# Optimization experiments

Measured on AMD Instinct MI355X. Metric: run time of the kernel, lower is better.

Reference implementation:

```python
import jax, jax.numpy as jnp
import numpy as np

B, S, D_MODEL = 2, 1024, 3072
HEADS, HEAD_DIM = 24, 128
EPS = 1e-6


def _rms_norm(x, w):
    # RMSNorm over last dim (head_dim), elementwise affine
    var = jnp.mean(jnp.square(x), axis=-1, keepdims=True)
    return x * jax.lax.rsqrt(var + EPS) * w


def _apply_rotary(x, freqs_cis):
    # x: [B, S, H, D]; freqs_cis: [S, 1, rot_dim] broadcasting over B via leading dims
    rot_dim = freqs_cis.shape[-1]
    xr, x_pass = x[..., :rot_dim], x[..., rot_dim:]
    cos_ = jnp.cos(freqs_cis).astype(x.dtype)
    sin_ = jnp.sin(freqs_cis).astype(x.dtype)
    x1, x2 = jnp.split(xr, 2, axis=-1)
    x_rot = jnp.concatenate((-x2, x1), axis=-1)
    return jnp.concatenate((xr * cos_ + x_rot * sin_, x_pass), axis=-1)


def setup_inputs() -> dict:
    key = jax.random.key(0)
    ks = jax.random.split(key, 8)
    inner = HEADS * HEAD_DIM
    scale = 1.0 / np.sqrt(D_MODEL)
    return {
        "hidden_states": jax.random.normal(ks[0], (B, S, D_MODEL), dtype=jnp.float32),
        "image_rotary_emb": jax.random.uniform(ks[1], (S, 1, HEAD_DIM), dtype=jnp.float32) * 6.283,
        "Wq": jax.random.normal(ks[2], (inner, D_MODEL), dtype=jnp.float32) * scale,
        "Wk": jax.random.normal(ks[3], (inner, D_MODEL), dtype=jnp.float32) * scale,
        "Wv": jax.random.normal(ks[4], (inner, D_MODEL), dtype=jnp.float32) * scale,
        "Wo": jax.random.normal(ks[5], (D_MODEL, inner), dtype=jnp.float32) * scale,
        "norm_q_w": jnp.ones((HEAD_DIM,), dtype=jnp.float32),
        "norm_k_w": jnp.ones((HEAD_DIM,), dtype=jnp.float32),
    }


def reference(hidden_states, image_rotary_emb, Wq, Wk, Wv, Wo, norm_q_w, norm_k_w):
    # QKV projections: [B,S,Dm] @ [Dm,inner] -> [B,S,H,Dh]
    q = jnp.einsum("bsd,ed->bse", hidden_states, Wq).reshape(B, S, HEADS, HEAD_DIM)
    k = jnp.einsum("bsd,ed->bse", hidden_states, Wk).reshape(B, S, HEADS, HEAD_DIM)
    v = jnp.einsum("bsd,ed->bse", hidden_states, Wv).reshape(B, S, HEADS, HEAD_DIM)
    # per-head RMSNorm on q/k
    q = _rms_norm(q, norm_q_w)
    k = _rms_norm(k, norm_k_w)
    # RoPE (Megatron rotate_half, full head dim rotated)
    q = _apply_rotary(q, image_rotary_emb)
    k = _apply_rotary(k, image_rotary_emb)
    # SDPA (non-causal, no mask): [B,H,S,S]
    scale = 1.0 / np.sqrt(HEAD_DIM)
    scores = jnp.einsum("bqhd,bkhd->bhqk", q, k) * scale
    attn = jax.nn.softmax(scores, axis=-1)
    out = jnp.einsum("bhqk,bkhd->bqhd", attn, v).reshape(B, S, HEADS * HEAD_DIM)
    return jnp.einsum("bse,de->bsd", out, Wo)
```

## Files before the change

kernel.cpp:

```cpp
#include <hip/hip_runtime.h>
#include <hip/hip_bf16.h>
#include <math.h>

#define B_   2
#define S_   1024
#define DM_  3072
#define H_   24
#define HD_  128
#define BH_  (B_*H_)
#define KDIM 3072
#define QSCALE 0.08838834764831845f

typedef __attribute__((ext_vector_type(8))) short short8;
typedef __attribute__((ext_vector_type(4))) float f32x4;

__device__ __forceinline__ unsigned short f2bf(float f) {
    union { float f; unsigned u; } v; v.f = f;
    unsigned r = v.u + 0x7fffu + ((v.u >> 16) & 1u);
    return (unsigned short)(r >> 16);
}

#define GLD_LDS16(gptr, ldsptr)                                                            \
    __builtin_amdgcn_global_load_lds(                                                      \
        (const __attribute__((address_space(1))) unsigned int*)(gptr),                     \
        (__attribute__((address_space(3))) unsigned int*)(ldsptr), 16, 0, 0)

#define SEG0 1572864
#define SEGW 2359296
#define SB1  (SEG0 + SEGW)
#define SB2  (SB1 + SEGW)
#define SB3  (SB2 + SEGW)
#define SB4  (SB3 + SEGW)
#define SB5  (SB4 + 32768)
#define CVT_BLOCKS 43136

__global__ __launch_bounds__(256) void cvt_all(const float* __restrict__ hs,
                                               const float* __restrict__ Wq,
                                               const float* __restrict__ Wk,
                                               const float* __restrict__ Wv,
                                               const float* __restrict__ Wo,
                                               const float* __restrict__ freqs,
                                               unsigned short* __restrict__ Xb,
                                               unsigned short* __restrict__ Wqkvb,
                                               unsigned short* __restrict__ Wob,
                                               float2* __restrict__ tab) {
    int i = blockIdx.x * 256 + threadIdx.x;
    const float* src;
    unsigned short* dst;
    int j;
    if (i < SEG0)      { src = hs; dst = Xb;              j = i; }
    else if (i < SB1)  { src = Wq; dst = Wqkvb;           j = i - SEG0; }
    else if (i < SB2)  { src = Wk; dst = Wqkvb + 9437184; j = i - SB1; }
    else if (i < SB3)  { src = Wv; dst = Wqkvb + 18874368; j = i - SB2; }
    else if (i < SB4)  { src = Wo; dst = Wob;             j = i - SB3; }
    else {
        j = i - SB4;
        float4 f = ((const float4*)freqs)[j];
        float4 lo = make_float4(cosf(f.x), sinf(f.x), cosf(f.y), sinf(f.y));
        float4 hi = make_float4(cosf(f.z), sinf(f.z), cosf(f.w), sinf(f.w));
        ((float4*)tab)[2 * j]     = lo;
        ((float4*)tab)[2 * j + 1] = hi;
        return;
    }
    float4 v = ((const float4*)src)[j];
    ushort4 o;
    o.x = f2bf(v.x); o.y = f2bf(v.y); o.z = f2bf(v.z); o.w = f2bf(v.w);
    ((ushort4*)dst)[j] = o;
}

template <int FUSED>
__global__ __launch_bounds__(256) void gemm_fused(const unsigned short* __restrict__ A,
                                                  const unsigned short* __restrict__ Bm,
                                                  float* __restrict__ C, int Ndim,
                                                  const float2* __restrict__ rtab,
                                                  const float* __restrict__ nqw,
                                                  const float* __restrict__ nkw,
                                                  unsigned short* __restrict__ Qb,
                                                  unsigned short* __restrict__ Kb,
                                                  unsigned short* __restrict__ Vtb) {
    __shared__ __align__(16) unsigned short As[128 * 64];
    __shared__ __align__(16) unsigned short Bs[128 * 64];
    __shared__ float pse[4][64];
    const int t = threadIdx.x;
    const int bx = blockIdx.x;
    const int m0 = blockIdx.y * 128, n0 = bx * 128;
    const int w = t >> 6, lane = t & 63, quad = lane >> 4, ln = lane & 15;
    const int wm = (w >> 1) * 64;
    const int p = w & 1;
    const int dj0 = p ? 32 : 0;
    const int rl = lane >> 3;
    const int gc = (lane & 7) ^ rl;
    const int cs = ln & 7;
    const int woff = (w == 1) ? 32 : (w == 2) ? -32 : 0;

    f32x4 acc[4][4];
#pragma unroll
    for (int i = 0; i < 4; ++i)
#pragma unroll
        for (int j = 0; j < 4; ++j) acc[i][j] = (f32x4){0.f, 0.f, 0.f, 0.f};

    const unsigned short* ga = &A[(long long)(m0 + w * 32 + rl) * KDIM + gc * 8];
    const unsigned short* gb = &Bm[(long long)(n0 + w * 32 + woff + rl) * KDIM + gc * 8];

    for (int kt = 0; kt < KDIM / 64; ++kt) {
#pragma unroll
        for (int c = 0; c < 4; ++c) {
            const int r0 = w * 32 + c * 8;
            GLD_LDS16(ga + (long long)(c * 8) * KDIM, &As[r0 * 64]);
            GLD_LDS16(gb + (long long)(c * 8) * KDIM, &Bs[r0 * 64]);
        }
        ga += 64; gb += 64;
        __syncthreads();
#pragma unroll
        for (int ks = 0; ks < 2; ++ks) {
            short8 a[4], b[4];
#pragma unroll
            for (int i = 0; i < 4; ++i) {
                int row = wm + i * 16 + ln;
                a[i] = *(const short8*)&As[row * 64 + (((ks * 4 + quad) ^ cs) << 3)];
            }
#pragma unroll
            for (int j = 0; j < 4; ++j) {
                int row = p * 64 + j * 16 + ln;
                b[j] = *(const short8*)&Bs[row * 64 + (((ks * 4 + quad) ^ cs) << 3)];
            }
#pragma unroll
            for (int i = 0; i < 4; ++i)
#pragma unroll
                for (int j = 0; j < 4; ++j)
                    acc[i][j] = __builtin_amdgcn_mfma_f32_16x16x32_bf16(a[i], b[j], acc[i][j], 0, 0, 0);
        }
        __syncthreads();
    }

    if (!FUSED) {
#pragma unroll
        for (int i = 0; i < 4; ++i)
#pragma unroll
            for (int reg = 0; reg < 4; ++reg) {
                int row = m0 + wm + i * 16 + quad * 4 + reg;
                float* crow = C + (long long)row * Ndim + n0 + ln;
                crow[dj0]      = acc[i][0][reg];
                crow[dj0 + 16] = acc[i][1][reg];
                crow[dj0 + 64] = acc[i][2][reg];
                crow[dj0 + 80] = acc[i][3][reg];
            }
        return;
    }
    const int region = bx / 24;
    const int h = bx % 24;
    if (region < 2) {
#pragma unroll
        for (int i = 0; i < 4; ++i)
#pragma unroll
            for (int reg = 0; reg < 4; ++reg) {
                float s = 0.f;
#pragma unroll
                for (int j = 0; j < 4; ++j) { float v = acc[i][j][reg]; s += v * v; }
#pragma unroll
                for (int off = 8; off; off >>= 1) s += __shfl_xor(s, off, 16);
                if (ln == 0) pse[w][i * 16 + quad * 4 + reg] = s;
            }
        __syncthreads();
        const float* nw = region ? nkw : nqw;
        unsigned short* outp = region ? Kb : Qb;
        const float scl = region ? 1.f : QSCALE;
        const float nw0  = nw[dj0 + ln],      nw1  = nw[dj0 + 16 + ln];
        const float nw64 = nw[dj0 + 64 + ln], nw80 = nw[dj0 + 80 + ln];
#pragma unroll
        for (int i = 0; i < 4; ++i)
#pragma unroll
            for (int reg = 0; reg < 4; ++reg) {
                const int idx = i * 16 + quad * 4 + reg;
                const float tot = pse[w][idx] + pse[w ^ 1][idx];
                const float rr = rsqrtf(tot * (1.f / 128.f) + 1e-6f);
                const int row = m0 + wm + idx;
                const int b = row >> 10, s = row & 1023;
                const long long ob = ((long long)(b * H_ + h) * S_ + s) * HD_;
                {
                    const int d1 = dj0 + ln;
                    float y1 = acc[i][0][reg] * rr * nw0;
                    float y2 = acc[i][2][reg] * rr * nw64;
                    float2 c1 = rtab[s * HD_ + d1], c2 = rtab[s * HD_ + d1 + 64];
                    outp[ob + d1]      = f2bf((y1 * c1.x - y2 * c1.y) * scl);
                    outp[ob + d1 + 64] = f2bf((y2 * c2.x + y1 * c2.y) * scl);
                }
                {
                    const int d1 = dj0 + 16 + ln;
                    float y1 = acc[i][1][reg] * rr * nw1;
                    float y2 = acc[i][3][reg] * rr * nw80;
                    float2 c1 = rtab[s * HD_ + d1], c2 = rtab[s * HD_ + d1 + 64];
                    outp[ob + d1]      = f2bf((y1 * c1.x - y2 * c1.y) * scl);
                    outp[ob + d1 + 64] = f2bf((y2 * c2.x + y1 * c2.y) * scl);
                }
            }
    } else {
#pragma unroll
        for (int i = 0; i < 4; ++i)
#pragma unroll
            for (int reg = 0; reg < 4; ++reg) {
                const int row = m0 + wm + i * 16 + quad * 4 + reg;
                const int b = row >> 10, s = row & 1023;
                const long long vb = (long long)(b * H_ + h) * HD_;
#pragma unroll
                for (int j = 0; j < 4; ++j) {
                    const int d = dj0 + (j & 1) * 16 + (j >> 1) * 64 + ln;
                    Vtb[(vb + d) * S_ + s] = f2bf(acc[i][j][reg]);
                }
            }
    }
}

__global__ __launch_bounds__(256) void attn(const unsigned short* __restrict__ Qb,
                                            const unsigned short* __restrict__ Kb,
                                            const unsigned short* __restrict__ Vtb,
                                            unsigned short* __restrict__ Ob) {
    __shared__ __align__(16) unsigned short Ks[64 * 128];
    __shared__ __align__(16) unsigned short Vts[128 * 64];
    __shared__ __align__(16) unsigned short Ps[4][16][72];
    const int bh = blockIdx.x, qt = blockIdx.y;
    const int t = threadIdx.x, w = t >> 6, lane = t & 63, quad = lane >> 4, ln = lane & 15;
    const int b = bh / H_, h = bh - b * H_;

    short8 qfrag[4];
    const long long qbase = ((long long)bh * S_ + qt * 64 + w * 16 + ln) * HD_;
#pragma unroll
    for (int ks = 0; ks < 4; ++ks)
        qfrag[ks] = *(const short8*)&Qb[qbase + ks * 32 + quad * 8];

    f32x4 o[8];
#pragma unroll
    for (int n = 0; n < 8; ++n) o[n] = (f32x4){0.f, 0.f, 0.f, 0.f};
    float l_run[4] = {0.f, 0.f, 0.f, 0.f};

    const int krow_l = lane >> 4, ksl = lane & 15;
    const int vrow_l = lane >> 3, vsl = lane & 7;

    for (int kt = 0; kt < S_ / 64; ++kt) {
        __syncthreads();
#pragma unroll
        for (int c = 0; c < 4; ++c) {
            {
                const int r = c * 16 + w * 4 + krow_l;
                const int gcn = ksl ^ (r & 15);
                GLD_LDS16(&Kb[((long long)bh * S_ + kt * 64 + r) * HD_ + gcn * 8],
                          &Ks[(c * 16 + w * 4) * 128]);
            }
            {
                const int r = c * 32 + w * 8 + vrow_l;
                const int gcn = vsl ^ (r & 7);
                GLD_LDS16(&Vtb[((long long)bh * HD_ + r) * S_ + kt * 64 + gcn * 8],
                          &Vts[(c * 32 + w * 8) * 64]);
            }
        }
        __syncthreads();
        f32x4 sj[4];
#pragma unroll
        for (int j = 0; j < 4; ++j) {
            f32x4 sa = (f32x4){0.f, 0.f, 0.f, 0.f};
#pragma unroll
            for (int ks = 0; ks < 4; ++ks) {
                const int row = j * 16 + ln;
                const int slot = (ks * 4 + quad) ^ (row & 15);
                short8 bb = *(const short8*)&Ks[row * 128 + slot * 8];
                sa = __builtin_amdgcn_mfma_f32_16x16x32_bf16(qfrag[ks], bb, sa, 0, 0, 0);
            }
            sj[j] = sa;
        }
#pragma unroll
        for (int r = 0; r < 4; ++r) {
            float sum = 0.f;
#pragma unroll
            for (int j = 0; j < 4; ++j) {
                float p = __expf(sj[j][r]);
                sj[j][r] = p;
                sum += p;
            }
#pragma unroll
            for (int off = 8; off; off >>= 1) sum += __shfl_xor(sum, off, 16);
            l_run[r] += sum;
        }
#pragma unroll
        for (int j = 0; j < 4; ++j)
#pragma unroll
            for (int r = 0; r < 4; ++r)
                Ps[w][quad * 4 + r][j * 16 + ln] = f2bf(sj[j][r]);
        __asm__ volatile("s_waitcnt lgkmcnt(0)" ::: "memory");
#pragma unroll
        for (int ks = 0; ks < 2; ++ks) {
            short8 pf = *(const short8*)&Ps[w][ln][ks * 32 + quad * 8];
#pragma unroll
            for (int n = 0; n < 8; ++n) {
                const int row = n * 16 + ln;
                const int slot = (ks * 4 + quad) ^ (row & 7);
                short8 vf = *(const short8*)&Vts[row * 64 + slot * 8];
                o[n] = __builtin_amdgcn_mfma_f32_16x16x32_bf16(pf, vf, o[n], 0, 0, 0);
            }
        }
    }
    float inv[4];
#pragma unroll
    for (int r = 0; r < 4; ++r) inv[r] = 1.f / l_run[r];
    const int row_s = qt * 64 + w * 16 + quad * 4;
#pragma unroll
    for (int n = 0; n < 8; ++n)
#pragma unroll
        for (int r = 0; r < 4; ++r) {
            long long off = ((long long)b * S_ + row_s + r) * DM_ + h * HD_ + n * 16 + ln;
            Ob[off] = f2bf(o[n][r] * inv[r]);
        }
}

extern "C" void kernel_launch(void* const* d_in, const int* in_sizes, int n_in,
                              void* d_out, int out_size, void* d_ws, size_t ws_size,
                              hipStream_t stream) {
    const float* hs    = (const float*)d_in[0];
    const float* freqs = (const float*)d_in[1];
    const float* Wq    = (const float*)d_in[2];
    const float* Wk    = (const float*)d_in[3];
    const float* Wv    = (const float*)d_in[4];
    const float* Wo    = (const float*)d_in[5];
    const float* nqw   = (const float*)d_in[6];
    const float* nkw   = (const float*)d_in[7];
    float* out = (float*)d_out;

    char* ws = (char*)d_ws;
    unsigned short* Xb    = (unsigned short*)(ws);
    unsigned short* Wqkvb = (unsigned short*)(ws + 12582912LL);
    unsigned short* Wob   = (unsigned short*)(ws + 69206016LL);
    unsigned short* Qb    = (unsigned short*)(ws + 88080384LL);
    unsigned short* Kb    = (unsigned short*)(ws + 100663296LL);
    unsigned short* Vtb   = (unsigned short*)(ws + 113246208LL);
    unsigned short* Ob    = (unsigned short*)(ws + 125829120LL);
    float2*         rtab  = (float2*)        (ws + 138412032LL);

    cvt_all<<<CVT_BLOCKS, 256, 0, stream>>>(hs, Wq, Wk, Wv, Wo, freqs,
                                            Xb, Wqkvb, Wob, rtab);
    gemm_fused<1><<<dim3(72, 16), 256, 0, stream>>>(Xb, Wqkvb, nullptr, 0,
                                                    rtab, nqw, nkw, Qb, Kb, Vtb);
    attn<<<dim3(BH_, S_ / 64), 256, 0, stream>>>(Qb, Kb, Vtb, Ob);
    gemm_fused<0><<<dim3(24, 16), 256, 0, stream>>>(Ob, Wob, out, DM_,
                                                    nullptr, nullptr, nullptr,
                                                    nullptr, nullptr, nullptr);
}
```

Measured before the change: 454.4 us.

## Swap grid axes for L2 reuse and use a 64-row tile for the output GEMM

Splits the templated GEMM into a QKV kernel and a separate output-projection kernel. The QKV and attention grids are transposed so consecutive blocks share the same weight tile or the same batch-head, which should improve L2 reuse of B rows and K/V. The output GEMM uses a 64x128 tile giving 768 blocks instead of 384, which fills the CUs better, at the cost of lower per-block arithmetic intensity.

```diff
diff --git a/kernel.cpp b/kernel.cpp
--- a/kernel.cpp
+++ b/kernel.cpp
@@ -68,22 +68,20 @@
     ((ushort4*)dst)[j] = o;
 }
 
-template <int FUSED>
-__global__ __launch_bounds__(256) void gemm_fused(const unsigned short* __restrict__ A,
-                                                  const unsigned short* __restrict__ Bm,
-                                                  float* __restrict__ C, int Ndim,
-                                                  const float2* __restrict__ rtab,
-                                                  const float* __restrict__ nqw,
-                                                  const float* __restrict__ nkw,
-                                                  unsigned short* __restrict__ Qb,
-                                                  unsigned short* __restrict__ Kb,
-                                                  unsigned short* __restrict__ Vtb) {
+__global__ __launch_bounds__(256) void gemm_qkv(const unsigned short* __restrict__ A,
+                                                const unsigned short* __restrict__ Bm,
+                                                const float2* __restrict__ rtab,
+                                                const float* __restrict__ nqw,
+                                                const float* __restrict__ nkw,
+                                                unsigned short* __restrict__ Qb,
+                                                unsigned short* __restrict__ Kb,
+                                                unsigned short* __restrict__ Vtb) {
     __shared__ __align__(16) unsigned short As[128 * 64];
     __shared__ __align__(16) unsigned short Bs[128 * 64];
     __shared__ float pse[4][64];
     const int t = threadIdx.x;
-    const int bx = blockIdx.x;
-    const int m0 = blockIdx.y * 128, n0 = bx * 128;
+    const int bx = blockIdx.y;
+    const int m0 = blockIdx.x * 128, n0 = bx * 128;
     const int w = t >> 6, lane = t & 63, quad = lane >> 4, ln = lane & 15;
     const int wm = (w >> 1) * 64;
     const int p = w & 1;
@@ -133,20 +131,6 @@
         __syncthreads();
     }
 
-    if (!FUSED) {
-#pragma unroll
-        for (int i = 0; i < 4; ++i)
-#pragma unroll
-            for (int reg = 0; reg < 4; ++reg) {
-                int row = m0 + wm + i * 16 + quad * 4 + reg;
-                float* crow = C + (long long)row * Ndim + n0 + ln;
-                crow[dj0]      = acc[i][0][reg];
-                crow[dj0 + 16] = acc[i][1][reg];
-                crow[dj0 + 64] = acc[i][2][reg];
-                crow[dj0 + 80] = acc[i][3][reg];
-            }
-        return;
-    }
     const int region = bx / 24;
     const int h = bx % 24;
     if (region < 2) {
@@ -211,6 +195,69 @@
     }
 }
 
+__global__ __launch_bounds__(256) void gemm_out(const unsigned short* __restrict__ A,
+                                                const unsigned short* __restrict__ Bm,
+                                                float* __restrict__ C, int Ndim) {
+    __shared__ __align__(16) unsigned short As[64 * 64];
+    __shared__ __align__(16) unsigned short Bs[128 * 64];
+    const int t = threadIdx.x;
+    const int m0 = blockIdx.x * 64, n0 = blockIdx.y * 128;
+    const int w = t >> 6, lane = t & 63, quad = lane >> 4, ln = lane & 15;
+    const int wm = (w >> 1) * 32, wn = (w & 1) * 64;
+    const int rl = lane >> 3;
+    const int gc = (lane & 7) ^ rl;
+    const int cs = ln & 7;
+
+    f32x4 acc[2][4];
+#pragma unroll
+    for (int i = 0; i < 2; ++i)
+#pragma unroll
+        for (int j = 0; j < 4; ++j) acc[i][j] = (f32x4){0.f, 0.f, 0.f, 0.f};
+
+    const unsigned short* ga = &A[(long long)(m0 + w * 16 + rl) * KDIM + gc * 8];
+    const unsigned short* gb = &Bm[(long long)(n0 + w * 32 + rl) * KDIM + gc * 8];
+
+    for (int kt = 0; kt < KDIM / 64; ++kt) {
+#pragma unroll
+        for (int c = 0; c < 2; ++c)
+            GLD_LDS16(ga + (long long)(c * 8) * KDIM, &As[(w * 16 + c * 8) * 64]);
+#pragma unroll
+        for (int c = 0; c < 4; ++c)
+            GLD_LDS16(gb + (long long)(c * 8) * KDIM, &Bs[(w * 32 + c * 8) * 64]);
+        ga += 64; gb += 64;
+        __syncthreads();
+#pragma unroll
+        for (int ks = 0; ks < 2; ++ks) {
+            short8 a[2], b[4];
+#pragma unroll
+            for (int i = 0; i < 2; ++i) {
+                int row = wm + i * 16 + ln;
+                a[i] = *(const short8*)&As[row * 64 + (((ks * 4 + quad) ^ cs) << 3)];
+            }
+#pragma unroll
+            for (int j = 0; j < 4; ++j) {
+                int row = wn + j * 16 + ln;
+                b[j] = *(const short8*)&Bs[row * 64 + (((ks * 4 + quad) ^ cs) << 3)];
+            }
+#pragma unroll
+            for (int i = 0; i < 2; ++i)
+#pragma unroll
+                for (int j = 0; j < 4; ++j)
+                    acc[i][j] = __builtin_amdgcn_mfma_f32_16x16x32_bf16(a[i], b[j], acc[i][j], 0, 0, 0);
+        }
+        __syncthreads();
+    }
+#pragma unroll
+    for (int i = 0; i < 2; ++i)
+#pragma unroll
+        for (int reg = 0; reg < 4; ++reg) {
+            int row = m0 + wm + i * 16 + quad * 4 + reg;
+            float* crow = C + (long long)row * Ndim + n0 + wn + ln;
+#pragma unroll
+            for (int j = 0; j < 4; ++j) crow[j * 16] = acc[i][j][reg];
+        }
+}
+
 __global__ __launch_bounds__(256) void attn(const unsigned short* __restrict__ Qb,
                                             const unsigned short* __restrict__ Kb,
                                             const unsigned short* __restrict__ Vtb,
@@ -218,7 +265,7 @@
     __shared__ __align__(16) unsigned short Ks[64 * 128];
     __shared__ __align__(16) unsigned short Vts[128 * 64];
     __shared__ __align__(16) unsigned short Ps[4][16][72];
-    const int bh = blockIdx.x, qt = blockIdx.y;
+    const int qt = blockIdx.x, bh = blockIdx.y;
     const int t = threadIdx.x, w = t >> 6, lane = t & 63, quad = lane >> 4, ln = lane & 15;
     const int b = bh / H_, h = bh - b * H_;
 
@@ -336,10 +383,7 @@
 
     cvt_all<<<CVT_BLOCKS, 256, 0, stream>>>(hs, Wq, Wk, Wv, Wo, freqs,
                                             Xb, Wqkvb, Wob, rtab);
-    gemm_fused<1><<<dim3(72, 16), 256, 0, stream>>>(Xb, Wqkvb, nullptr, 0,
-                                                    rtab, nqw, nkw, Qb, Kb, Vtb);
-    attn<<<dim3(BH_, S_ / 64), 256, 0, stream>>>(Qb, Kb, Vtb, Ob);
-    gemm_fused<0><<<dim3(24, 16), 256, 0, stream>>>(Ob, Wob, out, DM_,
-                                                    nullptr, nullptr, nullptr,
-                                                    nullptr, nullptr, nullptr);
-}
+    gemm_qkv<<<dim3(16, 72), 256, 0, stream>>>(Xb, Wqkvb, rtab, nqw, nkw, Qb, Kb, Vtb);
+    attn<<<dim3(16, BH_), 256, 0, stream>>>(Qb, Kb, Vtb, Ob);
+    gemm_out<<<dim3(32, 24), 256, 0, stream>>>(Ob, Wob, out, DM_);
+}
```

After: 457.8 us. No clear change (+0.8%).
